# Optimization experiments

Hardware: AMD Instinct MI355X
Metric: run time of the kernel (lower is better)

The kernel has to match this reference:

```python
import jax, jax.numpy as jnp
import numpy as np

NEG_CLAMP = -100.0  # torch F.binary_cross_entropy clamps log terms at -100


def _ccl_labels(fg):
    """4-connectivity connected-component labeling of a [H,W] bool mask.
    Labels are assigned in raster-scan first-encounter order, matching
    scipy.ndimage.label with the default structure. Background = 0.
    Implemented as min-index label propagation to a fixed point: each
    component ends up tagged with the min flat index of its pixels (its
    first raster-scan pixel), then roots are ranked by cumsum to get 1..num.
    """
    H, W = fg.shape
    INF = H * W  # sentinel larger than any flat index
    idx = jnp.arange(INF, dtype=jnp.int32).reshape(H, W)
    init = jnp.where(fg, idx, INF)

    def step(x):
        up = jnp.concatenate([x[1:], jnp.full((1, W), INF, x.dtype)], axis=0)
        down = jnp.concatenate([jnp.full((1, W), INF, x.dtype), x[:-1]], axis=0)
        left = jnp.concatenate([x[:, 1:], jnp.full((H, 1), INF, x.dtype)], axis=1)
        right = jnp.concatenate([jnp.full((H, 1), INF, x.dtype), x[:, :-1]], axis=1)
        m = jnp.minimum(jnp.minimum(up, down), jnp.minimum(left, right))
        return jnp.where(fg, jnp.minimum(x, m), INF)

    def cond(carry):
        return carry[1]

    def body(carry):
        x, _ = carry
        nx = step(x)
        return nx, jnp.any(nx != x)

    x, _ = jax.lax.while_loop(cond, body, (init, jnp.array(True)))

    flat = x.reshape(-1)
    fgf = fg.reshape(-1)
    # a pixel is the root of its component iff its propagated tag == its own index
    is_root = fgf & (flat == jnp.arange(INF, dtype=jnp.int32))
    rank = jnp.cumsum(is_root.astype(jnp.int32))  # rank[r] = scipy label of root r
    labels = jnp.where(fgf, rank[jnp.clip(flat, 0, INF - 1)], 0)
    return labels.reshape(H, W)


def _target_map(fg):
    """Replicates: labels == labels.flatten()[1:].argmax() + 1 (faithful to source,
    including its quirky use of argmax position as the selected label value)."""
    labels = _ccl_labels(fg)
    lf = labels.reshape(-1)
    v = jnp.argmax(lf[1:]) + 1  # first occurrence of max, like numpy argmax
    return (labels == v).astype(jnp.float32)


def setup_inputs() -> dict:
    key = jax.random.key(0)
    pred = jax.random.uniform(key, (32, 1, 512, 512), dtype=jnp.float32)
    return {"pred": pred}


def reference(pred):
    fg = pred[:, 0] >= 0.5  # [N,H,W] bool
    target = jax.vmap(_target_map)(fg)[:, None]  # [N,1,H,W] float
    logp = jnp.maximum(jnp.log(pred), NEG_CLAMP)
    log1mp = jnp.maximum(jnp.log1p(-pred), NEG_CLAMP)
    return -jnp.mean(target * logp + (1.0 - target) * log1mp)
```

## Files before the change

kernel.cpp:

```cpp
#include <hip/hip_runtime.h>
#include <math.h>

#define IMG_W 512
#define IMG_H 512
#define HW (IMG_W * IMG_H)
#define LOGHW 18
#define NIMG 32
#define NTOT (NIMG * HW)
#define TILE 64
#define TPI 64
#define NTILE (NIMG * TPI)
#define CPI 64
#define NSCHUNK (NIMG * CPI)
#define EDGE_N (NTILE * 64)
#define NPAIR (NIMG * 112)

__device__ __forceinline__ void uf_unite(int* L, int a, int b) {
    while (true) {
        int p = ((volatile int*)L)[a];
        while (p != a) { a = p; p = ((volatile int*)L)[a]; }
        p = ((volatile int*)L)[b];
        while (p != b) { b = p; p = ((volatile int*)L)[b]; }
        if (a == b) return;
        if (a < b) { int t = a; a = b; b = t; }
        int old = atomicMin(&L[a], b);
        if (old == a) return;
        a = old;
    }
}

__global__ __launch_bounds__(512) void k_local(const float* __restrict__ pred,
                                               int* __restrict__ L,
                                               float* __restrict__ partials,
                                               int* __restrict__ edges,
                                               unsigned int* __restrict__ counter) {
    __shared__ int lab[TILE * TILE];
    __shared__ float sred[512];
    int tile = blockIdx.x;
    int img = tile >> 6;
    int t = tile & (TPI - 1);
    int ty = t >> 3, tx = t & 7;
    int baseLocal = (ty * TILE) * IMG_W + tx * TILE;
    const float* pi = pred + ((size_t)img << LOGHW);
    int* Li = L + ((size_t)img << LOGHW);
    int tid = threadIdx.x;
    int lane = tid & 63, wave = tid >> 6;

    float acc = 0.0f;
#pragma unroll
    for (int j = 0; j < 8; j++) {
        int row = wave + j * 8;
        float p = pi[baseLocal + row * IMG_W + lane];
        acc += fmaxf(__logf(1.0f - p), -100.0f);
        bool fg = (p >= 0.5f);
        unsigned long long bal = __ballot(fg);
        unsigned long long starts = bal & ~(bal << 1);
        unsigned long long maskle =
            (lane == 63) ? ~0ULL : ((1ULL << (lane + 1)) - 1ULL);
        int lb = -1;
        if (fg) {
            unsigned long long pre = starts & maskle;
            lb = row * TILE + (63 - __builtin_clzll(pre));
        }
        lab[row * TILE + lane] = lb;
    }
    __syncthreads();
#pragma unroll
    for (int j = 0; j < 8; j++) {
        int row = wave + j * 8;
        if (row == 0) continue;
        int i = row * TILE + lane;
        bool c = (lab[i] >= 0) && (lab[i - TILE] >= 0);
        unsigned long long cb = __ballot(c);
        unsigned long long cs = cb & ~(cb << 1);
        if ((cs >> lane) & 1ULL) uf_unite(lab, i, i - TILE);
    }
    __syncthreads();
#pragma unroll
    for (int j = 0; j < 8; j++) {
        int row = wave + j * 8;
        int i = row * TILE + lane;
        bool fg = (lab[i] >= 0);
        unsigned long long bal = __ballot(fg);
        unsigned long long st = bal & ~(bal << 1);
        if ((st >> lane) & 1ULL) {
            int x = i, p = lab[x];
            while (p != x) {
                int g = lab[p];
                lab[x] = g;
                x = g;
                p = lab[x];
            }
            lab[i] = x;
        }
    }
    __syncthreads();
#pragma unroll
    for (int j = 0; j < 2; j++) {
        int i4 = (tid + j * 512) * 4;
        int ly = i4 >> 6, lx = i4 & 63;
        int4 o;
        int* op = (int*)&o;
#pragma unroll
        for (int k = 0; k < 4; k++) {
            int s = lab[i4 + k];
            if (s < 0) op[k] = -1;
            else {
                int r = lab[s];
                op[k] = baseLocal + (r >> 6) * IMG_W + (r & 63);
            }
        }
        *(int4*)(Li + baseLocal + ly * IMG_W + lx) = o;
    }
    if (tid < 256) {
        int e = tid >> 6;
        int q = tid & 63;
        int px = (e == 0) ? q
               : (e == 1) ? (63 * TILE + q)
               : (e == 2) ? (q * TILE)
               :            (q * TILE + 63);
        int s = lab[px];
        int val = -1;
        if (s >= 0) {
            int r = lab[s];
            val = baseLocal + (r >> 6) * IMG_W + (r & 63);
        }
        edges[e * EDGE_N + tile * 64 + q] = val;
    }
    sred[tid] = acc;
    __syncthreads();
    for (int s = 256; s > 0; s >>= 1) {
        if (tid < s) sred[tid] += sred[tid + s];
        __syncthreads();
    }
    if (tid == 0) partials[blockIdx.x] = sred[0];
    if (blockIdx.x == 0 && tid == 0) *counter = 0u;
}

__global__ __launch_bounds__(256) void k_border(const int* __restrict__ edges,
                                                int* __restrict__ L) {
    int gid = blockIdx.x * blockDim.x + threadIdx.x;
    int pair = gid >> 6;
    int lane = gid & 63;
    int a, b, img;
    if (pair < NIMG * 56) {
        img = pair / 56;
        int w = pair - img * 56;
        int ty = w / 7, tx = w - ty * 7;
        int tl = img * TPI + ty * 8 + tx;
        a = edges[3 * EDGE_N + tl * 64 + lane];
        b = edges[2 * EDGE_N + (tl + 1) * 64 + lane];
    } else {
        int p2 = pair - NIMG * 56;
        img = p2 / 56;
        int w = p2 - img * 56;
        int ty = w >> 3, tx = w & 7;
        int tu = img * TPI + ty * 8 + tx;
        a = edges[1 * EDGE_N + tu * 64 + lane];
        b = edges[0 * EDGE_N + (tu + 8) * 64 + lane];
    }
    bool c = (a >= 0) && (b >= 0);
    unsigned long long cb = __ballot(c);
    unsigned long long cs = cb & ~(cb << 1);
    if ((cs >> lane) & 1ULL)
        uf_unite(L + ((size_t)img << LOGHW), a, b);
}

__global__ __launch_bounds__(256) void k_stats(const int* __restrict__ L,
                                               int* __restrict__ cntArr,
                                               int* __restrict__ maxArr,
                                               int* __restrict__ minArr) {
    __shared__ int s1[256], s2[256], s3[256];
    int chunk = blockIdx.x;
    int img = chunk >> 6;
    int baseL = (chunk & 63) * 4096;
    const int* Li = L + ((size_t)img << LOGHW);
    int t = threadIdx.x;
    int cnt = 0, mx = -1, mn = HW;
#pragma unroll
    for (int j = 0; j < 4; j++) {
        int off = baseL + (t + j * 256) * 4;
        int4 l4 = *(const int4*)(Li + off);
        const int* lp = (const int*)&l4;
#pragma unroll
        for (int k = 0; k < 4; k++) {
            int local = off + k;
            int p = lp[k];
            bool root = (p == local);
            cnt += root ? 1 : 0;
            if (root && local > mx) mx = local;
            if (p >= 0 && local >= 1 && local < mn) mn = local;
        }
    }
    s1[t] = cnt; s2[t] = mx; s3[t] = mn;
    __syncthreads();
    for (int s = 128; s > 0; s >>= 1) {
        if (t < s) {
            s1[t] += s1[t + s];
            s2[t] = max(s2[t], s2[t + s]);
            s3[t] = min(s3[t], s3[t + s]);
        }
        __syncthreads();
    }
    if (t == 0) { cntArr[chunk] = s1[0]; maxArr[chunk] = s2[0]; minArr[chunk] = s3[0]; }
}

__global__ __launch_bounds__(256) void k_tail(const int* __restrict__ cntArr,
                                              const int* __restrict__ maxArr,
                                              const int* __restrict__ minArr,
                                              const int* __restrict__ L,
                                              const float* __restrict__ pred,
                                              const float* __restrict__ partials,
                                              float* __restrict__ corr,
                                              unsigned int* __restrict__ counter,
                                              float* __restrict__ out) {
    __shared__ int sc[256], sm[256], sn[256];
    __shared__ int sel_chunk, sel_base, result;
    __shared__ float sf[256];
    __shared__ double sd[256];
    __shared__ unsigned int oldc;
    int img = blockIdx.x, t = threadIdx.x;
    const int* Li = L + ((size_t)img << LOGHW);
    int cnt = (t < CPI) ? cntArr[img * CPI + t] : 0;
    sc[t] = cnt;
    sm[t] = (t < CPI) ? maxArr[img * CPI + t] : -1;
    sn[t] = (t < CPI) ? minArr[img * CPI + t] : HW;
    if (t == 0) result = -2;
    __syncthreads();
    for (int off = 1; off < 256; off <<= 1) {
        int v2 = (t >= off) ? sc[t - off] : 0;
        __syncthreads();
        sc[t] += v2;
        __syncthreads();
    }
    int num = sc[255];
    int inc = sc[t], exc = inc - cnt;
    for (int s = 128; s > 0; s >>= 1) {
        if (t < s) { sm[t] = max(sm[t], sm[t + s]); sn[t] = min(sn[t], sn[t + s]); }
        __syncthreads();
    }
    int last_root = sm[0], minFg = sn[0];
    int v;
    if (last_root >= 1) v = last_root;
    else if (last_root == 0) v = (minFg < HW) ? minFg : 1;
    else v = 1;
    if (v >= 1 && v <= num) {
        if (exc < v && v <= inc) { sel_chunk = t; sel_base = exc; }
        __syncthreads();
        int c = sel_chunk, base = sel_base;
        int baseL = c * 4096;
        int f[16];
        int sum = 0;
#pragma unroll
        for (int j = 0; j < 4; j++) {
            int off = baseL + t * 16 + j * 4;
            int4 l4 = *(const int4*)(Li + off);
            const int* lp = (const int*)&l4;
#pragma unroll
            for (int k = 0; k < 4; k++) {
                f[j * 4 + k] = (lp[k] == off + k) ? 1 : 0;
                sum += f[j * 4 + k];
            }
        }
        __syncthreads();
        sc[t] = sum;
        __syncthreads();
        for (int off = 1; off < 256; off <<= 1) {
            int v2 = (t >= off) ? sc[t - off] : 0;
            __syncthreads();
            sc[t] += v2;
            __syncthreads();
        }
        int exc2 = sc[t] - sum;
        int need = v - base;
        if (exc2 < need && need <= sc[t]) {
            int run = exc2;
#pragma unroll
            for (int k = 0; k < 16; k++) {
                run += f[k];
                if (run == need) { result = baseL + t * 16 + k; break; }
            }
        }
        __syncthreads();
    } else {
        __syncthreads();
    }
    int rvv = result;
    float blocksum = 0.0f;
    if (rvv >= 0) {
        const float* pi = pred + ((size_t)img << LOGHW);
        float acc = 0.0f;
        for (int it = 0; it < HW / 1024; it++) {
            int off = it * 1024 + t * 4;
            float4 p4 = *(const float4*)(pi + off);
            int4 l4 = *(const int4*)(Li + off);
            const float* pp = (const float*)&p4;
            const int* lp = (const int*)&l4;
#pragma unroll
            for (int k = 0; k < 4; k++) {
                int p = lp[k];
                if (p < 0) continue;
                int x = p, q = Li[x];
                while (q != x) { x = q; q = Li[x]; }
                if (x == rvv) {
                    float pr = pp[k];
                    acc += fmaxf(__logf(pr), -100.0f)
                         - fmaxf(__logf(1.0f - pr), -100.0f);
                }
            }
        }
        sf[t] = acc;
        __syncthreads();
        for (int s = 128; s > 0; s >>= 1) {
            if (t < s) sf[t] += sf[t + s];
            __syncthreads();
        }
        blocksum = sf[0];
    }
    if (t == 0) {
        __hip_atomic_store(&corr[img], blocksum, __ATOMIC_RELAXED,
                           __HIP_MEMORY_SCOPE_AGENT);
        oldc = __hip_atomic_fetch_add(counter, 1u, __ATOMIC_ACQ_REL,
                                      __HIP_MEMORY_SCOPE_AGENT);
    }
    __syncthreads();
    if (oldc != NIMG - 1) return;
    double acc = 0.0;
#pragma unroll
    for (int j = 0; j < 8; j++) acc += (double)partials[t + j * 256];
    if (t < NIMG)
        acc += (double)__hip_atomic_load(&corr[t], __ATOMIC_ACQUIRE,
                                         __HIP_MEMORY_SCOPE_AGENT);
    sd[t] = acc;
    __syncthreads();
    for (int s = 128; s > 0; s >>= 1) {
        if (t < s) sd[t] += sd[t + s];
        __syncthreads();
    }
    if (t == 0) out[0] = (float)(-sd[0] / (double)NTOT);
}

extern "C" void kernel_launch(void* const* d_in, const int* in_sizes, int n_in,
                              void* d_out, int out_size, void* d_ws, size_t ws_size,
                              hipStream_t stream) {
    const float* pred = (const float*)d_in[0];
    float* out = (float*)d_out;

    char* ws = (char*)d_ws;
    int* L = (int*)ws;
    int* edges = (int*)(ws + (size_t)NTOT * 4);
    int* cntArr = edges + 4 * EDGE_N;
    int* maxArr = cntArr + NSCHUNK;
    int* minArr = maxArr + NSCHUNK;
    float* partials = (float*)(minArr + NSCHUNK);
    float* corr = partials + NTILE;
    unsigned int* counter = (unsigned int*)(corr + NIMG);

    k_local<<<dim3(NTILE), dim3(512), 0, stream>>>(pred, L, partials, edges, counter);
    k_border<<<dim3(NPAIR * 64 / 256), dim3(256), 0, stream>>>(edges, L);
    k_stats<<<dim3(NSCHUNK), dim3(256), 0, stream>>>(L, cntArr, maxArr, minArr);
    k_tail<<<dim3(NIMG), dim3(256), 0, stream>>>(cntArr, maxArr, minArr, L, pred,
                                                 partials, corr, counter, out);
}
```

Before: 120.1 us.

## Process two tiles per block with prefetched loads and wave-shuffle reduction

Each k_local block now handles two adjacent 64x64 tiles. It loads both tiles' pixels into registers up front, so the second tile's global loads overlap the first tile's labeling. The shared-memory tree reduction is replaced by a wave shuffle reduction plus an 8-entry sum, and the partials array and the tail sum are halved to match. The trade-off is half as many blocks (1024), which lowers parallelism, plus extra register pressure from the 16 prefetched values.

```diff
diff --git a/kernel.cpp b/kernel.cpp
--- a/kernel.cpp
+++ b/kernel.cpp
@@ -10,6 +10,7 @@
 #define TILE 64
 #define TPI 64
 #define NTILE (NIMG * TPI)
+#define NBLK (NTILE / 2)
 #define CPI 64
 #define NSCHUNK (NIMG * CPI)
 #define EDGE_N (NTILE * 64)
@@ -35,105 +36,130 @@
                                                int* __restrict__ edges,
                                                unsigned int* __restrict__ counter) {
     __shared__ int lab[TILE * TILE];
-    __shared__ float sred[512];
-    int tile = blockIdx.x;
-    int img = tile >> 6;
-    int t = tile & (TPI - 1);
-    int ty = t >> 3, tx = t & 7;
-    int baseLocal = (ty * TILE) * IMG_W + tx * TILE;
+    __shared__ float wsum[8];
+    int tile0 = blockIdx.x * 2;
+    int img = tile0 >> 6;
     const float* pi = pred + ((size_t)img << LOGHW);
     int* Li = L + ((size_t)img << LOGHW);
     int tid = threadIdx.x;
     int lane = tid & 63, wave = tid >> 6;
 
-    float acc = 0.0f;
+    int baseL0, baseL1;
+    {
+        int t0 = tile0 & (TPI - 1);
+        baseL0 = ((t0 >> 3) * TILE) * IMG_W + (t0 & 7) * TILE;
+        int t1 = (tile0 + 1) & (TPI - 1);
+        baseL1 = ((t1 >> 3) * TILE) * IMG_W + (t1 & 7) * TILE;
+    }
+    float pvA[8], pvB[8];
 #pragma unroll
     for (int j = 0; j < 8; j++) {
         int row = wave + j * 8;
-        float p = pi[baseLocal + row * IMG_W + lane];
-        acc += fmaxf(__logf(1.0f - p), -100.0f);
-        bool fg = (p >= 0.5f);
-        unsigned long long bal = __ballot(fg);
-        unsigned long long starts = bal & ~(bal << 1);
-        unsigned long long maskle =
-            (lane == 63) ? ~0ULL : ((1ULL << (lane + 1)) - 1ULL);
-        int lb = -1;
-        if (fg) {
-            unsigned long long pre = starts & maskle;
-            lb = row * TILE + (63 - __builtin_clzll(pre));
-        }
-        lab[row * TILE + lane] = lb;
-    }
-    __syncthreads();
+        pvA[j] = pi[baseL0 + row * IMG_W + lane];
+    }
 #pragma unroll
     for (int j = 0; j < 8; j++) {
         int row = wave + j * 8;
-        if (row == 0) continue;
-        int i = row * TILE + lane;
-        bool c = (lab[i] >= 0) && (lab[i - TILE] >= 0);
-        unsigned long long cb = __ballot(c);
-        unsigned long long cs = cb & ~(cb << 1);
-        if ((cs >> lane) & 1ULL) uf_unite(lab, i, i - TILE);
-    }
-    __syncthreads();
-#pragma unroll
-    for (int j = 0; j < 8; j++) {
-        int row = wave + j * 8;
-        int i = row * TILE + lane;
-        bool fg = (lab[i] >= 0);
-        unsigned long long bal = __ballot(fg);
-        unsigned long long st = bal & ~(bal << 1);
-        if ((st >> lane) & 1ULL) {
-            int x = i, p = lab[x];
-            while (p != x) {
-                int g = lab[p];
-                lab[x] = g;
-                x = g;
-                p = lab[x];
-            }
-            lab[i] = x;
-        }
-    }
-    __syncthreads();
-#pragma unroll
-    for (int j = 0; j < 2; j++) {
-        int i4 = (tid + j * 512) * 4;
-        int ly = i4 >> 6, lx = i4 & 63;
-        int4 o;
-        int* op = (int*)&o;
-#pragma unroll
-        for (int k = 0; k < 4; k++) {
-            int s = lab[i4 + k];
-            if (s < 0) op[k] = -1;
-            else {
+        pvB[j] = pi[baseL1 + row * IMG_W + lane];
+    }
+
+    float acc = 0.0f;
+    unsigned long long maskle = (~0ULL) >> (63 - lane);
+
+    for (int it = 0; it < 2; it++) {
+        int tile = tile0 + it;
+        int baseLocal = it ? baseL1 : baseL0;
+#pragma unroll
+        for (int j = 0; j < 8; j++) {
+            int row = wave + j * 8;
+            float p = it ? pvB[j] : pvA[j];
+            acc += fmaxf(__logf(1.0f - p), -100.0f);
+            bool fg = (p >= 0.5f);
+            unsigned long long bal = __ballot(fg);
+            unsigned long long starts = bal & ~(bal << 1);
+            int lb = -1;
+            if (fg) {
+                unsigned long long pre = starts & maskle;
+                lb = row * TILE + (63 - __builtin_clzll(pre));
+            }
+            lab[row * TILE + lane] = lb;
+        }
+        __syncthreads();
+#pragma unroll
+        for (int j = 0; j < 8; j++) {
+            int row = wave + j * 8;
+            if (row == 0) continue;
+            int i = row * TILE + lane;
+            bool c = (lab[i] >= 0) && (lab[i - TILE] >= 0);
+            unsigned long long cb = __ballot(c);
+            unsigned long long cs = cb & ~(cb << 1);
+            if ((cs >> lane) & 1ULL) uf_unite(lab, i, i - TILE);
+        }
+        __syncthreads();
+#pragma unroll
+        for (int j = 0; j < 8; j++) {
+            int row = wave + j * 8;
+            int i = row * TILE + lane;
+            bool fg = (lab[i] >= 0);
+            unsigned long long bal = __ballot(fg);
+            unsigned long long st = bal & ~(bal << 1);
+            if ((st >> lane) & 1ULL) {
+                int x = i, p = lab[x];
+                while (p != x) {
+                    int g = lab[p];
+                    lab[x] = g;
+                    x = g;
+                    p = lab[x];
+                }
+                lab[i] = x;
+            }
+        }
+        __syncthreads();
+#pragma unroll
+        for (int j = 0; j < 2; j++) {
+            int i4 = (tid + j * 512) * 4;
+            int ly = i4 >> 6, lx = i4 & 63;
+            int4 o;
+            int* op = (int*)&o;
+#pragma unroll
+            for (int k = 0; k < 4; k++) {
+                int s = lab[i4 + k];
+                if (s < 0) op[k] = -1;
+                else {
+                    int r = lab[s];
+                    op[k] = baseLocal + (r >> 6) * IMG_W + (r & 63);
+                }
+            }
+            *(int4*)(Li + baseLocal + ly * IMG_W + lx) = o;
+        }
+        if (tid < 256) {
+            int e = tid >> 6;
+            int q = tid & 63;
+            int px = (e == 0) ? q
+                   : (e == 1) ? (63 * TILE + q)
+                   : (e == 2) ? (q * TILE)
+                   :            (q * TILE + 63);
+            int s = lab[px];
+            int val = -1;
+            if (s >= 0) {
                 int r = lab[s];
-                op[k] = baseLocal + (r >> 6) * IMG_W + (r & 63);
-            }
-        }
-        *(int4*)(Li + baseLocal + ly * IMG_W + lx) = o;
-    }
-    if (tid < 256) {
-        int e = tid >> 6;
-        int q = tid & 63;
-        int px = (e == 0) ? q
-               : (e == 1) ? (63 * TILE + q)
-               : (e == 2) ? (q * TILE)
-               :            (q * TILE + 63);
-        int s = lab[px];
-        int val = -1;
-        if (s >= 0) {
-            int r = lab[s];
-            val = baseLocal + (r >> 6) * IMG_W + (r & 63);
-        }
-        edges[e * EDGE_N + tile * 64 + q] = val;
-    }
-    sred[tid] = acc;
-    __syncthreads();
-    for (int s = 256; s > 0; s >>= 1) {
-        if (tid < s) sred[tid] += sred[tid + s];
-        __syncthreads();
-    }
-    if (tid == 0) partials[blockIdx.x] = sred[0];
+                val = baseLocal + (r >> 6) * IMG_W + (r & 63);
+            }
+            edges[e * EDGE_N + tile * 64 + q] = val;
+        }
+        __syncthreads();
+    }
+#pragma unroll
+    for (int off = 32; off > 0; off >>= 1)
+        acc += __shfl_down(acc, off, 64);
+    if (lane == 0) wsum[wave] = acc;
+    __syncthreads();
+    if (tid == 0) {
+        float s = 0.0f;
+#pragma unroll
+        for (int w = 0; w < 8; w++) s += wsum[w];
+        partials[blockIdx.x] = s;
+    }
     if (blockIdx.x == 0 && tid == 0) *counter = 0u;
 }
 
@@ -327,7 +353,7 @@
     if (oldc != NIMG - 1) return;
     double acc = 0.0;
 #pragma unroll
-    for (int j = 0; j < 8; j++) acc += (double)partials[t + j * 256];
+    for (int j = 0; j < 4; j++) acc += (double)partials[t + j * 256];
     if (t < NIMG)
         acc += (double)__hip_atomic_load(&corr[t], __ATOMIC_ACQUIRE,
                                          __HIP_MEMORY_SCOPE_AGENT);
@@ -353,10 +379,10 @@
     int* maxArr = cntArr + NSCHUNK;
     int* minArr = maxArr + NSCHUNK;
     float* partials = (float*)(minArr + NSCHUNK);
-    float* corr = partials + NTILE;
+    float* corr = partials + NBLK;
     unsigned int* counter = (unsigned int*)(corr + NIMG);
 
-    k_local<<<dim3(NTILE), dim3(512), 0, stream>>>(pred, L, partials, edges, counter);
+    k_local<<<dim3(NBLK), dim3(512), 0, stream>>>(pred, L, partials, edges, counter);
     k_border<<<dim3(NPAIR * 64 / 256), dim3(256), 0, stream>>>(edges, L);
     k_stats<<<dim3(NSCHUNK), dim3(256), 0, stream>>>(L, cntArr, maxArr, minArr);
     k_tail<<<dim3(NIMG), dim3(256), 0, stream>>>(cntArr, maxArr, minArr, L, pred,
```

New measurement: 135.8 us. +13.1%, slower.

## Fuse stats and tail kernels via per-image last-block atomic counters

Applied to the files above, without the earlier changes.

Merges the per-chunk statistics kernel and the per-image tail kernel into one launch. The last block to finish each image, detected through a per-image atomic counter, performs the tail selection and correction work, and a global counter still picks the final reducer. The shared-memory tree reductions in the stats phase are replaced with wave shuffles. This removes one kernel launch and its inter-kernel gap. In exchange the tail work runs on whichever block finishes last per image, and the kernel now relies on atomic ordering across blocks.

```diff
diff --git a/kernel.cpp b/kernel.cpp
--- a/kernel.cpp
+++ b/kernel.cpp
@@ -33,7 +33,7 @@
                                                int* __restrict__ L,
                                                float* __restrict__ partials,
                                                int* __restrict__ edges,
-                                               unsigned int* __restrict__ counter) {
+                                               unsigned int* __restrict__ counters) {
     __shared__ int lab[TILE * TILE];
     __shared__ float sred[512];
     int tile = blockIdx.x;
@@ -134,7 +134,7 @@
         __syncthreads();
     }
     if (tid == 0) partials[blockIdx.x] = sred[0];
-    if (blockIdx.x == 0 && tid == 0) *counter = 0u;
+    if (blockIdx.x == 0 && tid <= NIMG) counters[tid] = 0u;
 }
 
 __global__ __launch_bounds__(256) void k_border(const int* __restrict__ edges,
@@ -166,16 +166,24 @@
         uf_unite(L + ((size_t)img << LOGHW), a, b);
 }
 
-__global__ __launch_bounds__(256) void k_stats(const int* __restrict__ L,
-                                               int* __restrict__ cntArr,
-                                               int* __restrict__ maxArr,
-                                               int* __restrict__ minArr) {
-    __shared__ int s1[256], s2[256], s3[256];
+__global__ __launch_bounds__(256) void k_stats_tail(
+        const int* __restrict__ L, const float* __restrict__ pred,
+        int* __restrict__ cntArr, int* __restrict__ maxArr,
+        int* __restrict__ minArr, const float* __restrict__ partials,
+        float* __restrict__ corr, unsigned int* __restrict__ counters,
+        float* __restrict__ out) {
+    __shared__ int sc[256], sm[256], sn[256];
+    __shared__ int swc[4], swx[4], swn[4];
+    __shared__ int sel_chunk, sel_base, result;
+    __shared__ float sf[256];
+    __shared__ double sd[256];
+    __shared__ unsigned int oldc, oldg;
     int chunk = blockIdx.x;
     int img = chunk >> 6;
     int baseL = (chunk & 63) * 4096;
     const int* Li = L + ((size_t)img << LOGHW);
     int t = threadIdx.x;
+    int lane = t & 63, wv = t >> 6;
     int cnt = 0, mx = -1, mn = HW;
 #pragma unroll
     for (int j = 0; j < 4; j++) {
@@ -192,39 +200,37 @@
             if (p >= 0 && local >= 1 && local < mn) mn = local;
         }
     }
-    s1[t] = cnt; s2[t] = mx; s3[t] = mn;
-    __syncthreads();
-    for (int s = 128; s > 0; s >>= 1) {
-        if (t < s) {
-            s1[t] += s1[t + s];
-            s2[t] = max(s2[t], s2[t + s]);
-            s3[t] = min(s3[t], s3[t + s]);
-        }
-        __syncthreads();
-    }
-    if (t == 0) { cntArr[chunk] = s1[0]; maxArr[chunk] = s2[0]; minArr[chunk] = s3[0]; }
-}
-
-__global__ __launch_bounds__(256) void k_tail(const int* __restrict__ cntArr,
-                                              const int* __restrict__ maxArr,
-                                              const int* __restrict__ minArr,
-                                              const int* __restrict__ L,
-                                              const float* __restrict__ pred,
-                                              const float* __restrict__ partials,
-                                              float* __restrict__ corr,
-                                              unsigned int* __restrict__ counter,
-                                              float* __restrict__ out) {
-    __shared__ int sc[256], sm[256], sn[256];
-    __shared__ int sel_chunk, sel_base, result;
-    __shared__ float sf[256];
-    __shared__ double sd[256];
-    __shared__ unsigned int oldc;
-    int img = blockIdx.x, t = threadIdx.x;
-    const int* Li = L + ((size_t)img << LOGHW);
-    int cnt = (t < CPI) ? cntArr[img * CPI + t] : 0;
-    sc[t] = cnt;
-    sm[t] = (t < CPI) ? maxArr[img * CPI + t] : -1;
-    sn[t] = (t < CPI) ? minArr[img * CPI + t] : HW;
+#pragma unroll
+    for (int off = 32; off > 0; off >>= 1) {
+        cnt += __shfl_down(cnt, off, 64);
+        mx = max(mx, __shfl_down(mx, off, 64));
+        mn = min(mn, __shfl_down(mn, off, 64));
+    }
+    if (lane == 0) { swc[wv] = cnt; swx[wv] = mx; swn[wv] = mn; }
+    __syncthreads();
+    if (t == 0) {
+        int c = swc[0] + swc[1] + swc[2] + swc[3];
+        int x = max(max(swx[0], swx[1]), max(swx[2], swx[3]));
+        int n = min(min(swn[0], swn[1]), min(swn[2], swn[3]));
+        __hip_atomic_store(&cntArr[chunk], c, __ATOMIC_RELAXED,
+                           __HIP_MEMORY_SCOPE_AGENT);
+        __hip_atomic_store(&maxArr[chunk], x, __ATOMIC_RELAXED,
+                           __HIP_MEMORY_SCOPE_AGENT);
+        __hip_atomic_store(&minArr[chunk], n, __ATOMIC_RELAXED,
+                           __HIP_MEMORY_SCOPE_AGENT);
+        oldc = __hip_atomic_fetch_add(&counters[img], 1u, __ATOMIC_ACQ_REL,
+                                      __HIP_MEMORY_SCOPE_AGENT);
+    }
+    __syncthreads();
+    if (oldc != CPI - 1) return;
+
+    int c0 = (t < CPI) ? __hip_atomic_load(&cntArr[img * CPI + t],
+                  __ATOMIC_ACQUIRE, __HIP_MEMORY_SCOPE_AGENT) : 0;
+    sc[t] = c0;
+    sm[t] = (t < CPI) ? __hip_atomic_load(&maxArr[img * CPI + t],
+                  __ATOMIC_ACQUIRE, __HIP_MEMORY_SCOPE_AGENT) : -1;
+    sn[t] = (t < CPI) ? __hip_atomic_load(&minArr[img * CPI + t],
+                  __ATOMIC_ACQUIRE, __HIP_MEMORY_SCOPE_AGENT) : HW;
     if (t == 0) result = -2;
     __syncthreads();
     for (int off = 1; off < 256; off <<= 1) {
@@ -234,7 +240,7 @@
         __syncthreads();
     }
     int num = sc[255];
-    int inc = sc[t], exc = inc - cnt;
+    int inc = sc[t], exc = inc - c0;
     for (int s = 128; s > 0; s >>= 1) {
         if (t < s) { sm[t] = max(sm[t], sm[t + s]); sn[t] = min(sn[t], sn[t + s]); }
         __syncthreads();
@@ -248,12 +254,12 @@
         if (exc < v && v <= inc) { sel_chunk = t; sel_base = exc; }
         __syncthreads();
         int c = sel_chunk, base = sel_base;
-        int baseL = c * 4096;
+        int bL = c * 4096;
         int f[16];
         int sum = 0;
 #pragma unroll
         for (int j = 0; j < 4; j++) {
-            int off = baseL + t * 16 + j * 4;
+            int off = bL + t * 16 + j * 4;
             int4 l4 = *(const int4*)(Li + off);
             const int* lp = (const int*)&l4;
 #pragma unroll
@@ -278,7 +284,7 @@
 #pragma unroll
             for (int k = 0; k < 16; k++) {
                 run += f[k];
-                if (run == need) { result = baseL + t * 16 + k; break; }
+                if (run == need) { result = bL + t * 16 + k; break; }
             }
         }
         __syncthreads();
@@ -320,11 +326,11 @@
     if (t == 0) {
         __hip_atomic_store(&corr[img], blocksum, __ATOMIC_RELAXED,
                            __HIP_MEMORY_SCOPE_AGENT);
-        oldc = __hip_atomic_fetch_add(counter, 1u, __ATOMIC_ACQ_REL,
+        oldg = __hip_atomic_fetch_add(&counters[NIMG], 1u, __ATOMIC_ACQ_REL,
                                       __HIP_MEMORY_SCOPE_AGENT);
     }
     __syncthreads();
-    if (oldc != NIMG - 1) return;
+    if (oldg != NIMG - 1) return;
     double acc = 0.0;
 #pragma unroll
     for (int j = 0; j < 8; j++) acc += (double)partials[t + j * 256];
@@ -354,11 +360,12 @@
     int* minArr = maxArr + NSCHUNK;
     float* partials = (float*)(minArr + NSCHUNK);
     float* corr = partials + NTILE;
-    unsigned int* counter = (unsigned int*)(corr + NIMG);
-
-    k_local<<<dim3(NTILE), dim3(512), 0, stream>>>(pred, L, partials, edges, counter);
+    unsigned int* counters = (unsigned int*)(corr + NIMG);
+
+    k_local<<<dim3(NTILE), dim3(512), 0, stream>>>(pred, L, partials, edges,
+                                                   counters);
     k_border<<<dim3(NPAIR * 64 / 256), dim3(256), 0, stream>>>(edges, L);
-    k_stats<<<dim3(NSCHUNK), dim3(256), 0, stream>>>(L, cntArr, maxArr, minArr);
-    k_tail<<<dim3(NIMG), dim3(256), 0, stream>>>(cntArr, maxArr, minArr, L, pred,
-                                                 partials, corr, counter, out);
-}
+    k_stats_tail<<<dim3(NSCHUNK), dim3(256), 0, stream>>>(L, pred, cntArr, maxArr,
+                                                          minArr, partials, corr,
+                                                          counters, out);
+}
```

New measurement: 165.4 us. 1.38x slower.
